# Kernel optimization log

Hardware: AMD Instinct MI355X
Metric: run time of the kernel (lower is better)

The kernel has to match this reference:

```python
import jax, jax.numpy as jnp
import numpy as np

N = 8192
M = 16
F_NODE = 128
HID = 512


def setup_inputs() -> dict:
    key = jax.random.key(0)
    ks = jax.random.split(key, 10)
    node_in_fea = jax.random.normal(ks[0], (N, F_NODE), dtype=jnp.float32)
    edge_fea_idx = jax.random.randint(ks[1], (N, M), 0, N, dtype=jnp.int64)
    s_emb = 1.0 / np.sqrt(F_NODE)
    s_h = 1.0 / np.sqrt(HID)
    W_emb = jax.random.uniform(ks[2], (F_NODE, HID), jnp.float32, -s_emb, s_emb)
    b_emb = jax.random.uniform(ks[3], (HID,), jnp.float32, -s_emb, s_emb)
    W1 = jax.random.uniform(ks[4], (HID, HID), jnp.float32, -s_h, s_h)
    b1 = jax.random.uniform(ks[5], (HID,), jnp.float32, -s_h, s_h)
    W2 = jax.random.uniform(ks[6], (HID, HID), jnp.float32, -s_h, s_h)
    b2 = jax.random.uniform(ks[7], (HID,), jnp.float32, -s_h, s_h)
    W3 = jax.random.uniform(ks[8], (HID, HID), jnp.float32, -s_h, s_h)
    b3 = jax.random.uniform(ks[9], (HID,), jnp.float32, -s_h, s_h)
    return {"node_in_fea": node_in_fea, "edge_fea_idx": edge_fea_idx,
            "W_emb": W_emb, "b_emb": b_emb, "W1": W1, "b1": b1,
            "W2": W2, "b2": b2, "W3": W3, "b3": b3}


def _normalized_adj(edge_fea_idx, n):
    # build dense adjacency: adj[i, j] += 1 for each valid neighbor j of i
    rows = jnp.broadcast_to(jnp.arange(n)[:, None], edge_fea_idx.shape)
    valid = edge_fea_idx >= 0  # -1 marks invalid neighbor
    cols = jnp.where(valid, edge_fea_idx, 0)
    vals = valid.astype(jnp.float32)
    adj = jnp.zeros((n, n), jnp.float32).at[rows.reshape(-1), cols.reshape(-1)].add(vals.reshape(-1))
    # add self-loops, symmetric normalization D^{-1/2} A D^{-1/2}
    adj = adj + jnp.eye(n, dtype=jnp.float32)
    deg = jnp.sum(adj, axis=1)
    d_inv_sqrt = jnp.where(deg > 0, deg ** -0.5, 0.0)
    return adj * d_inv_sqrt[:, None] * d_inv_sqrt[None, :]


def reference(node_in_fea, edge_fea_idx, W_emb, b_emb, W1, b1, W2, b2, W3, b3):
    adj = _normalized_adj(edge_fea_idx, node_in_fea.shape[0])
    x = node_in_fea @ W_emb + b_emb          # (N, HID)
    x = jax.nn.relu((adj @ x) @ W1 + b1)     # gcn1 + relu
    x = jax.nn.relu((adj @ x) @ W2 + b2)     # gcn2 + relu
    x = (adj @ x) @ W3 + b3                  # gcn3 (no relu)
    return x
```

## Files before the change

kernel.cpp:

```cpp
#include <hip/hip_runtime.h>
#include <stdint.h>

#define NN 8192
#define MM 16
#define FN 128
#define HH 512

typedef unsigned short u16;
typedef unsigned int u32;
typedef __bf16 bf16;
typedef __bf16 bf16x8 __attribute__((ext_vector_type(8)));
typedef float f32x4 __attribute__((ext_vector_type(4)));

__device__ __forceinline__ void gld_lds16(const u16* g, u16* l) {
  __builtin_amdgcn_global_load_lds(
      (const __attribute__((address_space(1))) void*)g,
      (__attribute__((address_space(3))) void*)l, 16, 0, 0);
}

__device__ __forceinline__ int probe_f32(const u16* w) {
  int lane = threadIdx.x & 63;
  int e = (w[2 * lane] >> 7) & 0xFF;
  unsigned long long m = __ballot(!(e == 0 || (e >= 90 && e <= 140)));
  return __popcll(m) >= 8;
}
__device__ __forceinline__ int probe_i64(const u32* w) {
  int lane = threadIdx.x & 63;
  unsigned long long m = __ballot(lane < 32 && w[2 * lane + 1] != 0);
  return m == 0;
}

__global__ __launch_bounds__(256) void prep_kernel(
    const u16* __restrict__ node, const u32* __restrict__ idxw,
    const void* __restrict__ Wemb, const void* __restrict__ b0,
    const void* __restrict__ W1, const void* __restrict__ b1,
    const void* __restrict__ W2, const void* __restrict__ b2,
    const void* __restrict__ W3, const void* __restrict__ b3,
    float* __restrict__ dis, u16* __restrict__ biasBF, u16* __restrict__ TWemb,
    u16* __restrict__ TW1, u16* __restrict__ TW2, u16* __restrict__ TW3) {
  const int f32in = probe_f32(node);
  const int i64 = probe_i64(idxw);
  const int bid = blockIdx.x, tid = threadIdx.x;
  if (bid < 32) {
    const int i = bid * 256 + tid;
    const int* idx = (const int*)idxw;
    int c = 1;
#pragma unroll
    for (int e = 0; e < MM; ++e) c += (idx[(i * MM + e) << i64] >= 0) ? 1 : 0;
    dis[i] = rsqrtf((float)c);
  } else if (bid < 40) {
    const int id = (bid - 32) * 256 + tid;
    const int q = id >> 9;
    const void* src = q == 0 ? b0 : q == 1 ? b1 : q == 2 ? b2 : b3;
    const int off = id & (HH - 1);
    bf16 v = f32in ? (bf16)((const float*)src)[off] : ((const bf16*)src)[off];
    biasBF[id] = *(u16*)&v;
  } else {
    int t = bid - 40;
    const void* W;
    u16* T;
    int K, tt;
    if (t < 64) {
      W = Wemb; T = TWemb; K = FN; tt = t;
    } else {
      int q = (t - 64) >> 8;
      tt = (t - 64) & 255;
      K = HH;
      W = q == 0 ? W1 : q == 1 ? W2 : W3;
      T = q == 0 ? TW1 : q == 1 ? TW2 : TW3;
    }
    const int k0 = (tt >> 4) * 32, n0 = (tt & 15) * 32;
    __shared__ u16 sm[32 * 33];
    const int tx = tid & 31, ty = tid >> 5;
#pragma unroll
    for (int r = ty; r < 32; r += 8) {
      size_t src = (size_t)(k0 + r) * HH + n0 + tx;
      bf16 v = f32in ? (bf16)((const float*)W)[src] : ((const bf16*)W)[src];
      sm[r * 33 + tx] = *(u16*)&v;
    }
    __syncthreads();
#pragma unroll
    for (int r = ty; r < 32; r += 8)
      T[(size_t)(n0 + r) * K + k0 + tx] = sm[tx * 33 + r];
  }
}

template <bool RELU>
__device__ __forceinline__ void gemm_tile(const void* __restrict__ A, int K,
                                          int af32, const u16* __restrict__ Bt,
                                          const u16* __restrict__ bias,
                                          int rtile, int ctile, int outf32,
                                          void* __restrict__ C, u16* As,
                                          u16* Bs) {
  const int tid = threadIdx.x;
  const int wave = tid >> 6, lane = tid & 63;
  const int wr = wave >> 1, wc = wave & 1;
  const int quad = lane >> 4, l16 = lane & 15;
  f32x4 acc[2][4] = {};

  int arow[2], agc[2], brow[4], bgc[4];
#pragma unroll
  for (int i = 0; i < 2; ++i) {
    int c = i * 256 + tid;
    arow[i] = c >> 3;
    agc[i] = (c & 7) ^ (arow[i] & 7);
  }
#pragma unroll
  for (int i = 0; i < 4; ++i) {
    int c = i * 256 + tid;
    brow[i] = c >> 3;
    bgc[i] = (c & 7) ^ (brow[i] & 7);
  }
  u16* AsW = As + wave * 512;
  u16* BsW = Bs + wave * 512;

  for (int k0 = 0; k0 < K; k0 += 64) {
    __syncthreads();
    if (af32) {
      const float* Af = (const float*)A;
      bf16x8 v[2];
#pragma unroll
      for (int i = 0; i < 2; ++i) {
        const float* p = &Af[(size_t)(rtile * 64 + arow[i]) * K + k0 + agc[i] * 8];
        f32x4 x0 = *(const f32x4*)p, x1 = *(const f32x4*)(p + 4);
#pragma unroll
        for (int t = 0; t < 4; ++t) {
          v[i][t] = (bf16)x0[t];
          v[i][4 + t] = (bf16)x1[t];
        }
      }
#pragma unroll
      for (int i = 0; i < 2; ++i) *(bf16x8*)&As[(i * 256 + tid) * 8] = v[i];
    } else {
      const u16* Ab = (const u16*)A;
#pragma unroll
      for (int i = 0; i < 2; ++i)
        gld_lds16(&Ab[(size_t)(rtile * 64 + arow[i]) * K + k0 + agc[i] * 8],
                  AsW + i * 2048);
    }
#pragma unroll
    for (int i = 0; i < 4; ++i)
      gld_lds16(&Bt[(size_t)(ctile * 128 + brow[i]) * K + k0 + bgc[i] * 8],
                BsW + i * 2048);
    __syncthreads();
#pragma unroll
    for (int h = 0; h < 2; ++h) {
      bf16x8 af[2], bfr[4];
#pragma unroll
      for (int i = 0; i < 2; ++i) {
        int r = wr * 32 + i * 16 + l16;
        int cc = (h * 4 + quad) ^ (r & 7);
        af[i] = *(const bf16x8*)&As[r * 64 + cc * 8];
      }
#pragma unroll
      for (int j = 0; j < 4; ++j) {
        int n = wc * 64 + j * 16 + l16;
        int cc = (h * 4 + quad) ^ (n & 7);
        bfr[j] = *(const bf16x8*)&Bs[n * 64 + cc * 8];
      }
#pragma unroll
      for (int i = 0; i < 2; ++i)
#pragma unroll
        for (int j = 0; j < 4; ++j)
          acc[i][j] = __builtin_amdgcn_mfma_f32_16x16x32_bf16(af[i], bfr[j],
                                                              acc[i][j], 0, 0, 0);
    }
  }

  const int crow0 = rtile * 64 + wr * 32 + quad * 4;
  const int ccol0 = ctile * 128 + wc * 64 + l16;
#pragma unroll
  for (int j = 0; j < 4; ++j) {
    const int col = ccol0 + j * 16;
    const float bv = (float)(*(const bf16*)&bias[col]);
#pragma unroll
    for (int i = 0; i < 2; ++i)
#pragma unroll
      for (int r = 0; r < 4; ++r) {
        float v = acc[i][j][r] + bv;
        if (RELU) v = fmaxf(v, 0.0f);
        size_t off = (size_t)(crow0 + i * 16 + r) * HH + col;
        if (outf32) {
          ((float*)C)[off] = v;
        } else {
          bf16 o = (bf16)v;
          ((u16*)C)[off] = *(u16*)&o;
        }
      }
  }
}

__global__ __launch_bounds__(256) void gemm_emb(const void* __restrict__ A,
                                                const u16* __restrict__ Bt,
                                                const u16* __restrict__ bias,
                                                u16* __restrict__ C) {
  __shared__ __align__(16) u16 As[64 * 64];
  __shared__ __align__(16) u16 Bs[128 * 64];
  const int af32 = probe_f32((const u16*)A);
  gemm_tile<false>(A, FN, af32, Bt, bias, blockIdx.x, blockIdx.y, 0, C, As, Bs);
}

template <bool RELU, bool FINAL>
__global__ __launch_bounds__(256) void gemm_main(const u16* __restrict__ A,
                                                 const u16* __restrict__ Bt,
                                                 const u16* __restrict__ bias,
                                                 const u16* __restrict__ nodeprobe,
                                                 void* __restrict__ C) {
  __shared__ __align__(16) u16 As[64 * 64];
  __shared__ __align__(16) u16 Bs[128 * 64];
  int outf32 = 0;
  if (FINAL) outf32 = probe_f32(nodeprobe);
  gemm_tile<RELU>(A, HH, 0, Bt, bias, blockIdx.x, blockIdx.y, outf32, C, As, Bs);
}

__global__ __launch_bounds__(256) void agg_kernel(const u16* __restrict__ x,
                                                  const u32* __restrict__ idxw,
                                                  const float* __restrict__ dis,
                                                  u16* __restrict__ y) {
  const int i64 = probe_i64(idxw);
  const int* idx = (const int*)idxw;
  const int node = blockIdx.x * 4 + (threadIdx.x >> 6);
  const int lane = threadIdx.x & 63;
  const int c0 = lane * 8;
  const float wi = dis[node];
  float acc[8];
  bf16x8 xs = *(const bf16x8*)&x[(size_t)node * HH + c0];
#pragma unroll
  for (int t = 0; t < 8; ++t) acc[t] = wi * wi * (float)xs[t];
#pragma unroll
  for (int e = 0; e < MM; ++e) {
    const int j = idx[(node * MM + e) << i64];
    if (j >= 0) {
      const float w = wi * dis[j];
      bf16x8 v = *(const bf16x8*)&x[(size_t)j * HH + c0];
#pragma unroll
      for (int t = 0; t < 8; ++t) acc[t] += w * (float)v[t];
    }
  }
  bf16x8 o;
#pragma unroll
  for (int t = 0; t < 8; ++t) o[t] = (bf16)acc[t];
  *(bf16x8*)&y[(size_t)node * HH + c0] = o;
}

extern "C" void kernel_launch(void* const* d_in, const int* in_sizes, int n_in,
                              void* d_out, int out_size, void* d_ws, size_t ws_size,
                              hipStream_t stream) {
  const u16* node = (const u16*)d_in[0];
  const u32* idxw = (const u32*)d_in[1];
  const void* Wemb = d_in[2];
  const void* bemb = d_in[3];
  const void* W1 = d_in[4];
  const void* b1 = d_in[5];
  const void* W2 = d_in[6];
  const void* b2 = d_in[7];
  const void* W3 = d_in[8];
  const void* b3 = d_in[9];

  char* p = (char*)d_ws;
  float* dis = (float*)p;  p += NN * sizeof(float);
  u16* biasBF = (u16*)p;   p += 4 * HH * sizeof(u16);
  u16* TWemb = (u16*)p;    p += (size_t)HH * FN * 2;
  u16* TW1 = (u16*)p;      p += (size_t)HH * HH * 2;
  u16* TW2 = (u16*)p;      p += (size_t)HH * HH * 2;
  u16* TW3 = (u16*)p;      p += (size_t)HH * HH * 2;
  u16* xA = (u16*)p;
  u16* xO = (u16*)d_out;

  prep_kernel<<<872, 256, 0, stream>>>(node, idxw, Wemb, bemb, W1, b1, W2, b2,
                                       W3, b3, dis, biasBF, TWemb, TW1, TW2, TW3);
  gemm_emb<<<dim3(128, 4), 256, 0, stream>>>(node, TWemb, biasBF, xO);
  agg_kernel<<<NN / 4, 256, 0, stream>>>(xO, idxw, dis, xA);
  gemm_main<true, false>
      <<<dim3(128, 4), 256, 0, stream>>>(xA, TW1, biasBF + HH, node, xO);
  agg_kernel<<<NN / 4, 256, 0, stream>>>(xO, idxw, dis, xA);
  gemm_main<true, false>
      <<<dim3(128, 4), 256, 0, stream>>>(xA, TW2, biasBF + 2 * HH, node, xO);
  agg_kernel<<<NN / 4, 256, 0, stream>>>(xO, idxw, dis, xA);
  gemm_main<false, true>
      <<<dim3(128, 4), 256, 0, stream>>>(xA, TW3, biasBF + 3 * HH, node, d_out);
}
```

Measured before the change: 180.0 us.

## Overlap weight prep with embedding GEMM and remap aggregation blocks by column strip

Splits the prep kernel so only the embedding weight transpose and bias run first. The degree normalization, remaining biases and W1-W3 transposes now run as extra blocks inside the embedding GEMM launch, overlapping them with GEMM work. The aggregation kernel is also remapped so each block covers 16 nodes across one 128-column strip, with four nodes per wave, to change gather locality. This adds branchy heterogeneous blocks to the GEMM launch, which can cause load imbalance.

Result: faster. 170.4 us (-5.3%).

```diff
diff --git a/kernel.cpp b/kernel.cpp
--- a/kernel.cpp
+++ b/kernel.cpp
@@ -30,58 +30,36 @@
   return m == 0;
 }
 
-__global__ __launch_bounds__(256) void prep_kernel(
-    const u16* __restrict__ node, const u32* __restrict__ idxw,
-    const void* __restrict__ Wemb, const void* __restrict__ b0,
-    const void* __restrict__ W1, const void* __restrict__ b1,
-    const void* __restrict__ W2, const void* __restrict__ b2,
-    const void* __restrict__ W3, const void* __restrict__ b3,
-    float* __restrict__ dis, u16* __restrict__ biasBF, u16* __restrict__ TWemb,
-    u16* __restrict__ TW1, u16* __restrict__ TW2, u16* __restrict__ TW3) {
+__device__ __forceinline__ void transpose_tile(const void* __restrict__ W,
+                                               u16* __restrict__ T, int K,
+                                               int tt, int f32in, u16* sm) {
+  const int k0 = (tt >> 4) * 32, n0 = (tt & 15) * 32;
+  const int tx = threadIdx.x & 31, ty = threadIdx.x >> 5;
+#pragma unroll
+  for (int r = ty; r < 32; r += 8) {
+    size_t src = (size_t)(k0 + r) * HH + n0 + tx;
+    bf16 v = f32in ? (bf16)((const float*)W)[src] : ((const bf16*)W)[src];
+    sm[r * 33 + tx] = *(u16*)&v;
+  }
+  __syncthreads();
+#pragma unroll
+  for (int r = ty; r < 32; r += 8)
+    T[(size_t)(n0 + r) * K + k0 + tx] = sm[tx * 33 + r];
+}
+
+__global__ __launch_bounds__(256) void prepA_kernel(
+    const u16* __restrict__ node, const void* __restrict__ Wemb,
+    const void* __restrict__ b0, u16* __restrict__ biasBF,
+    u16* __restrict__ TWemb) {
+  __shared__ u16 sm[32 * 33];
   const int f32in = probe_f32(node);
-  const int i64 = probe_i64(idxw);
   const int bid = blockIdx.x, tid = threadIdx.x;
-  if (bid < 32) {
-    const int i = bid * 256 + tid;
-    const int* idx = (const int*)idxw;
-    int c = 1;
-#pragma unroll
-    for (int e = 0; e < MM; ++e) c += (idx[(i * MM + e) << i64] >= 0) ? 1 : 0;
-    dis[i] = rsqrtf((float)c);
-  } else if (bid < 40) {
-    const int id = (bid - 32) * 256 + tid;
-    const int q = id >> 9;
-    const void* src = q == 0 ? b0 : q == 1 ? b1 : q == 2 ? b2 : b3;
-    const int off = id & (HH - 1);
-    bf16 v = f32in ? (bf16)((const float*)src)[off] : ((const bf16*)src)[off];
-    biasBF[id] = *(u16*)&v;
+  if (bid < 2) {
+    const int off = bid * 256 + tid;
+    bf16 v = f32in ? (bf16)((const float*)b0)[off] : ((const bf16*)b0)[off];
+    biasBF[off] = *(u16*)&v;
   } else {
-    int t = bid - 40;
-    const void* W;
-    u16* T;
-    int K, tt;
-    if (t < 64) {
-      W = Wemb; T = TWemb; K = FN; tt = t;
-    } else {
-      int q = (t - 64) >> 8;
-      tt = (t - 64) & 255;
-      K = HH;
-      W = q == 0 ? W1 : q == 1 ? W2 : W3;
-      T = q == 0 ? TW1 : q == 1 ? TW2 : TW3;
-    }
-    const int k0 = (tt >> 4) * 32, n0 = (tt & 15) * 32;
-    __shared__ u16 sm[32 * 33];
-    const int tx = tid & 31, ty = tid >> 5;
-#pragma unroll
-    for (int r = ty; r < 32; r += 8) {
-      size_t src = (size_t)(k0 + r) * HH + n0 + tx;
-      bf16 v = f32in ? (bf16)((const float*)W)[src] : ((const bf16*)W)[src];
-      sm[r * 33 + tx] = *(u16*)&v;
-    }
-    __syncthreads();
-#pragma unroll
-    for (int r = ty; r < 32; r += 8)
-      T[(size_t)(n0 + r) * K + k0 + tx] = sm[tx * 33 + r];
+    transpose_tile(Wemb, TWemb, FN, bid - 2, f32in, sm);
   }
 }
 
@@ -190,14 +168,46 @@
   }
 }
 
-__global__ __launch_bounds__(256) void gemm_emb(const void* __restrict__ A,
-                                                const u16* __restrict__ Bt,
-                                                const u16* __restrict__ bias,
-                                                u16* __restrict__ C) {
+__global__ __launch_bounds__(256) void emb_plus_kernel(
+    const u16* __restrict__ node, const u32* __restrict__ idxw,
+    const void* __restrict__ W1, const void* __restrict__ b1,
+    const void* __restrict__ W2, const void* __restrict__ b2,
+    const void* __restrict__ W3, const void* __restrict__ b3,
+    const u16* __restrict__ TWemb, const u16* __restrict__ biasBF,
+    float* __restrict__ dis, u16* __restrict__ biasBF_w,
+    u16* __restrict__ TW1, u16* __restrict__ TW2, u16* __restrict__ TW3,
+    u16* __restrict__ xout) {
   __shared__ __align__(16) u16 As[64 * 64];
   __shared__ __align__(16) u16 Bs[128 * 64];
-  const int af32 = probe_f32((const u16*)A);
-  gemm_tile<false>(A, FN, af32, Bt, bias, blockIdx.x, blockIdx.y, 0, C, As, Bs);
+  const int bid = blockIdx.x, tid = threadIdx.x;
+  if (bid < 512) {
+    const int af32 = probe_f32(node);
+    gemm_tile<false>(node, FN, af32, TWemb, biasBF, bid >> 2, bid & 3, 0, xout,
+                     As, Bs);
+  } else if (bid < 544) {
+    const int i64 = probe_i64(idxw);
+    const int* idx = (const int*)idxw;
+    const int i = (bid - 512) * 256 + tid;
+    int c = 1;
+#pragma unroll
+    for (int e = 0; e < MM; ++e) c += (idx[(i * MM + e) << i64] >= 0) ? 1 : 0;
+    dis[i] = rsqrtf((float)c);
+  } else if (bid < 550) {
+    const int f32in = probe_f32(node);
+    const int id = (bid - 544) * 256 + tid;
+    const int q = id >> 9;
+    const void* src = q == 0 ? b1 : q == 1 ? b2 : b3;
+    const int off = id & (HH - 1);
+    bf16 v = f32in ? (bf16)((const float*)src)[off] : ((const bf16*)src)[off];
+    biasBF_w[HH + id] = *(u16*)&v;
+  } else {
+    const int f32in = probe_f32(node);
+    const int t = bid - 550;
+    const int q = t >> 8, tt = t & 255;
+    const void* W = q == 0 ? W1 : q == 1 ? W2 : W3;
+    u16* T = q == 0 ? TW1 : q == 1 ? TW2 : TW3;
+    transpose_tile(W, T, HH, tt, f32in, As);
+  }
 }
 
 template <bool RELU, bool FINAL>
@@ -219,9 +229,12 @@
                                                   u16* __restrict__ y) {
   const int i64 = probe_i64(idxw);
   const int* idx = (const int*)idxw;
-  const int node = blockIdx.x * 4 + (threadIdx.x >> 6);
-  const int lane = threadIdx.x & 63;
-  const int c0 = lane * 8;
+  const int b = blockIdx.x;
+  const int strip = (b & 7) >> 1;
+  const int grp = (b >> 3) * 2 + (b & 1);
+  const int wave = threadIdx.x >> 6, lane = threadIdx.x & 63;
+  const int node = grp * 16 + wave * 4 + (lane >> 4);
+  const int c0 = strip * 128 + (lane & 15) * 8;
   const float wi = dis[node];
   float acc[8];
   bf16x8 xs = *(const bf16x8*)&x[(size_t)node * HH + c0];
@@ -267,9 +280,10 @@
   u16* xA = (u16*)p;
   u16* xO = (u16*)d_out;
 
-  prep_kernel<<<872, 256, 0, stream>>>(node, idxw, Wemb, bemb, W1, b1, W2, b2,
-                                       W3, b3, dis, biasBF, TWemb, TW1, TW2, TW3);
-  gemm_emb<<<dim3(128, 4), 256, 0, stream>>>(node, TWemb, biasBF, xO);
+  prepA_kernel<<<66, 256, 0, stream>>>(node, Wemb, bemb, biasBF, TWemb);
+  emb_plus_kernel<<<1318, 256, 0, stream>>>(node, idxw, W1, b1, W2, b2, W3, b3,
+                                            TWemb, biasBF, dis, biasBF, TW1,
+                                            TW2, TW3, xO);
   agg_kernel<<<NN / 4, 256, 0, stream>>>(xO, idxw, dis, xA);
   gemm_main<true, false>
       <<<dim3(128, 4), 256, 0, stream>>>(xA, TW1, biasBF + HH, node, xO);
```
